# Optimization experiments

Measured on AMD Instinct MI355X. Metric: run time of the kernel, lower is better.

Reference implementation:

```python
import jax, jax.numpy as jnp
import numpy as np


def setup_inputs() -> dict:
    key = jax.random.key(0)
    k1, k2, k3, k4, k5 = jax.random.split(key, 5)
    B, C, H, W = 32, 256, 64, 64
    R = 16  # reduction -> hidden = C // R = 16
    hid = C // R
    return {
        "x": jax.random.normal(k1, (B, C, H, W), dtype=jnp.float32),
        "w1": jax.random.normal(k2, (hid, 1, 1, 1), dtype=jnp.float32) * 0.1,
        "b1": jax.random.normal(k3, (hid,), dtype=jnp.float32) * 0.1,
        "w2": jax.random.normal(k4, (C, hid, 1, 1), dtype=jnp.float32) * 0.1,
        "b2": jax.random.normal(k5, (C,), dtype=jnp.float32) * 0.1,
    }


def reference(x, w1, b1, w2, b2):
    # PositionalAveragePooling: mean over channel dim -> [B, 1, H, W]
    s = jnp.mean(x, axis=1)  # [B, H, W]
    # conv1 (1 -> hid, 1x1): per-position scalar times weight vector + bias
    w1v = w1[:, 0, 0, 0]  # [hid]
    h = jax.nn.relu(s[:, None, :, :] * w1v[None, :, None, None]
                    + b1[None, :, None, None])  # [B, hid, H, W]
    # conv2 (hid -> C, 1x1): pointwise matmul over channel dim
    w2m = w2[:, :, 0, 0]  # [C, hid]
    scale = jax.nn.sigmoid(jnp.einsum("bkhw,ck->bchw", h, w2m)
                           + b2[None, :, None, None])  # [B, C, H, W]
    return x * scale
```

## Files before the change

kernel.cpp:

```cpp
#include <hip/hip_runtime.h>

#define NB 32
#define NC 256
#define NH 64
#define NW 64
#define NK 16
#define HW (NH * NW)

__device__ __forceinline__ float fsig(float z) {
    return __builtin_amdgcn_rcpf(1.0f + __expf(-z));
}

__global__ __launch_bounds__(256, 4) void pse_kernel(
    const float* __restrict__ x,
    const float* __restrict__ w1,
    const float* __restrict__ b1,
    const float* __restrict__ w2,
    const float* __restrict__ b2,
    float* __restrict__ out)
{
    __shared__ float  w2t[NK][NC];
    __shared__ float4 part[16][17];
    __shared__ float4 hv4[NK][16];
    __shared__ float4 s4[16];

    const int t  = threadIdx.x;
    const int cg = t >> 4;
    const int q  = t & 15;

    const int bh = blockIdx.x;
    const int b  = bh >> 6;
    const int h  = bh & 63;

    const size_t base = (size_t)b * NC * HW + (size_t)h * NW;
    const float* __restrict__ xp = x + base;
    float* __restrict__ op       = out + base;

    {
        const float4* w2v = reinterpret_cast<const float4*>(w2);
        #pragma unroll
        for (int r = 0; r < 4; ++r) {
            const int idx = t + (r << 8);
            const float4 v = w2v[idx];
            const int c  = idx >> 2;
            const int k0 = (idx & 3) << 2;
            w2t[k0 + 0][c] = v.x;
            w2t[k0 + 1][c] = v.y;
            w2t[k0 + 2][c] = v.z;
            w2t[k0 + 3][c] = v.w;
        }
    }

    {
        const float* xr = xp + (size_t)(cg << 4) * HW + (q << 2);
        float4 pacc = make_float4(0.f, 0.f, 0.f, 0.f);
        #pragma unroll
        for (int i = 0; i < 16; ++i) {
            const float4 v = *reinterpret_cast<const float4*>(xr + (size_t)i * HW);
            pacc.x += v.x; pacc.y += v.y; pacc.z += v.z; pacc.w += v.w;
        }
        part[cg][q] = pacc;
    }
    __syncthreads();

    if (t < 16) {
        float4 s = make_float4(0.f, 0.f, 0.f, 0.f);
        #pragma unroll
        for (int i = 0; i < 16; ++i) {
            const float4 v = part[i][t];
            s.x += v.x; s.y += v.y; s.z += v.z; s.w += v.w;
        }
        const float inv = 1.0f / (float)NC;
        s.x *= inv; s.y *= inv; s.z *= inv; s.w *= inv;
        s4[t] = s;
    }
    __syncthreads();

    {
        const float4 s  = s4[q];
        const float w1k = w1[cg];
        const float b1k = b1[cg];
        float4 hvv;
        hvv.x = fmaxf(fmaf(s.x, w1k, b1k), 0.f);
        hvv.y = fmaxf(fmaf(s.y, w1k, b1k), 0.f);
        hvv.z = fmaxf(fmaf(s.z, w1k, b1k), 0.f);
        hvv.w = fmaxf(fmaf(s.w, w1k, b1k), 0.f);
        hv4[cg][q] = hvv;
    }
    __syncthreads();

    float4 acc[16];
    #pragma unroll
    for (int i = 0; i < 16; ++i) {
        const float bb = b2[(cg << 4) + i];
        acc[i] = make_float4(bb, bb, bb, bb);
    }

    #pragma unroll
    for (int k = 0; k < NK; ++k) {
        const float4 hk = hv4[k][q];
        const float4* wr = reinterpret_cast<const float4*>(&w2t[k][cg << 4]);
        const float4 wa = wr[0], wb = wr[1], wc = wr[2], wd = wr[3];
        const float wv[16] = {wa.x, wa.y, wa.z, wa.w, wb.x, wb.y, wb.z, wb.w,
                              wc.x, wc.y, wc.z, wc.w, wd.x, wd.y, wd.z, wd.w};
        #pragma unroll
        for (int i = 0; i < 16; ++i) {
            acc[i].x = fmaf(hk.x, wv[i], acc[i].x);
            acc[i].y = fmaf(hk.y, wv[i], acc[i].y);
            acc[i].z = fmaf(hk.z, wv[i], acc[i].z);
            acc[i].w = fmaf(hk.w, wv[i], acc[i].w);
        }
    }

    #pragma unroll
    for (int i = 0; i < 16; ++i) {
        const size_t off = (size_t)((cg << 4) + i) * HW + (q << 2);
        const float4 xv = *reinterpret_cast<const float4*>(xp + off);
        const float4 a  = acc[i];
        float4 r;
        r.x = xv.x * fsig(a.x);
        r.y = xv.y * fsig(a.y);
        r.z = xv.z * fsig(a.z);
        r.w = xv.w * fsig(a.w);
        *reinterpret_cast<float4*>(op + off) = r;
    }
}

extern "C" void kernel_launch(void* const* d_in, const int* in_sizes, int n_in,
                              void* d_out, int out_size, void* d_ws, size_t ws_size,
                              hipStream_t stream) {
    const float* x  = (const float*)d_in[0];
    const float* w1 = (const float*)d_in[1];
    const float* b1 = (const float*)d_in[2];
    const float* w2 = (const float*)d_in[3];
    const float* b2 = (const float*)d_in[4];
    float* out = (float*)d_out;

    dim3 grid(NB * NH);
    dim3 block(256);
    hipLaunchKernelGGL(pse_kernel, grid, block, 0, stream, x, w1, b1, w2, b2, out);
}
```

Before: 255.8 us.

## Keep x tile in registers, use nontemporal loads/stores, split accumulation in halves

Result: faster. 237.7 us (-7.1%).

```diff
diff --git a/kernel.cpp b/kernel.cpp
--- a/kernel.cpp
+++ b/kernel.cpp
@@ -6,6 +6,8 @@
 #define NW 64
 #define NK 16
 #define HW (NH * NW)
+
+typedef float f32x4 __attribute__((ext_vector_type(4)));
 
 __device__ __forceinline__ float fsig(float z) {
     return __builtin_amdgcn_rcpf(1.0f + __expf(-z));
@@ -19,10 +21,11 @@
     const float* __restrict__ b2,
     float* __restrict__ out)
 {
-    __shared__ float  w2t[NK][NC];
-    __shared__ float4 part[16][17];
-    __shared__ float4 hv4[NK][16];
-    __shared__ float4 s4[16];
+    __shared__ float w2t[NK][NC + 4];
+    __shared__ f32x4 part[16][17];
+    __shared__ f32x4 hv4[NK][16];
+    __shared__ f32x4 s4[16];
+    __shared__ float b2s[NC];
 
     const int t  = threadIdx.x;
     const int cg = t >> 4;
@@ -35,13 +38,20 @@
     const size_t base = (size_t)b * NC * HW + (size_t)h * NW;
     const float* __restrict__ xp = x + base;
     float* __restrict__ op       = out + base;
+    const float* __restrict__ xr = xp + (size_t)(cg << 4) * HW + (q << 2);
+
+    f32x4 xv[16];
+    #pragma unroll
+    for (int i = 0; i < 16; ++i)
+        xv[i] = __builtin_nontemporal_load(
+            reinterpret_cast<const f32x4*>(xr + (size_t)i * HW));
 
     {
-        const float4* w2v = reinterpret_cast<const float4*>(w2);
+        const f32x4* __restrict__ w2v = reinterpret_cast<const f32x4*>(w2);
         #pragma unroll
         for (int r = 0; r < 4; ++r) {
             const int idx = t + (r << 8);
-            const float4 v = w2v[idx];
+            const f32x4 v = w2v[idx];
             const int c  = idx >> 2;
             const int k0 = (idx & 3) << 2;
             w2t[k0 + 0][c] = v.x;
@@ -49,38 +59,31 @@
             w2t[k0 + 2][c] = v.z;
             w2t[k0 + 3][c] = v.w;
         }
+        b2s[t] = b2[t];
     }
 
     {
-        const float* xr = xp + (size_t)(cg << 4) * HW + (q << 2);
-        float4 pacc = make_float4(0.f, 0.f, 0.f, 0.f);
+        f32x4 p = (f32x4)(0.f);
         #pragma unroll
-        for (int i = 0; i < 16; ++i) {
-            const float4 v = *reinterpret_cast<const float4*>(xr + (size_t)i * HW);
-            pacc.x += v.x; pacc.y += v.y; pacc.z += v.z; pacc.w += v.w;
-        }
-        part[cg][q] = pacc;
+        for (int i = 0; i < 16; ++i) p += xv[i];
+        part[cg][q] = p;
     }
     __syncthreads();
 
     if (t < 16) {
-        float4 s = make_float4(0.f, 0.f, 0.f, 0.f);
+        f32x4 s = (f32x4)(0.f);
         #pragma unroll
-        for (int i = 0; i < 16; ++i) {
-            const float4 v = part[i][t];
-            s.x += v.x; s.y += v.y; s.z += v.z; s.w += v.w;
-        }
-        const float inv = 1.0f / (float)NC;
-        s.x *= inv; s.y *= inv; s.z *= inv; s.w *= inv;
+        for (int i = 0; i < 16; ++i) s += part[i][t];
+        s *= (1.0f / (float)NC);
         s4[t] = s;
     }
     __syncthreads();
 
     {
-        const float4 s  = s4[q];
+        const f32x4 s  = s4[q];
         const float w1k = w1[cg];
         const float b1k = b1[cg];
-        float4 hvv;
+        f32x4 hvv;
         hvv.x = fmaxf(fmaf(s.x, w1k, b1k), 0.f);
         hvv.y = fmaxf(fmaf(s.y, w1k, b1k), 0.f);
         hvv.z = fmaxf(fmaf(s.z, w1k, b1k), 0.f);
@@ -89,40 +92,42 @@
     }
     __syncthreads();
 
-    float4 acc[16];
     #pragma unroll
-    for (int i = 0; i < 16; ++i) {
-        const float bb = b2[(cg << 4) + i];
-        acc[i] = make_float4(bb, bb, bb, bb);
-    }
+    for (int half = 0; half < 2; ++half) {
+        const int c0 = (cg << 4) + (half << 3);
 
-    #pragma unroll
-    for (int k = 0; k < NK; ++k) {
-        const float4 hk = hv4[k][q];
-        const float4* wr = reinterpret_cast<const float4*>(&w2t[k][cg << 4]);
-        const float4 wa = wr[0], wb = wr[1], wc = wr[2], wd = wr[3];
-        const float wv[16] = {wa.x, wa.y, wa.z, wa.w, wb.x, wb.y, wb.z, wb.w,
-                              wc.x, wc.y, wc.z, wc.w, wd.x, wd.y, wd.z, wd.w};
+        f32x4 acc[8];
         #pragma unroll
-        for (int i = 0; i < 16; ++i) {
-            acc[i].x = fmaf(hk.x, wv[i], acc[i].x);
-            acc[i].y = fmaf(hk.y, wv[i], acc[i].y);
-            acc[i].z = fmaf(hk.z, wv[i], acc[i].z);
-            acc[i].w = fmaf(hk.w, wv[i], acc[i].w);
+        for (int j = 0; j < 8; ++j) acc[j] = (f32x4)(b2s[c0 + j]);
+
+        #pragma unroll
+        for (int k = 0; k < NK; ++k) {
+            const f32x4 hk = hv4[k][q];
+            const f32x4* __restrict__ wr =
+                reinterpret_cast<const f32x4*>(&w2t[k][c0]);
+            const f32x4 wa = wr[0], wb = wr[1];
+            const float wv[8] = {wa.x, wa.y, wa.z, wa.w, wb.x, wb.y, wb.z, wb.w};
+            #pragma unroll
+            for (int j = 0; j < 8; ++j) {
+                acc[j].x = fmaf(hk.x, wv[j], acc[j].x);
+                acc[j].y = fmaf(hk.y, wv[j], acc[j].y);
+                acc[j].z = fmaf(hk.z, wv[j], acc[j].z);
+                acc[j].w = fmaf(hk.w, wv[j], acc[j].w);
+            }
         }
-    }
 
-    #pragma unroll
-    for (int i = 0; i < 16; ++i) {
-        const size_t off = (size_t)((cg << 4) + i) * HW + (q << 2);
-        const float4 xv = *reinterpret_cast<const float4*>(xp + off);
-        const float4 a  = acc[i];
-        float4 r;
-        r.x = xv.x * fsig(a.x);
-        r.y = xv.y * fsig(a.y);
-        r.z = xv.z * fsig(a.z);
-        r.w = xv.w * fsig(a.w);
-        *reinterpret_cast<float4*>(op + off) = r;
+        #pragma unroll
+        for (int j = 0; j < 8; ++j) {
+            const int i = (half << 3) + j;
+            const f32x4 xvv = xv[i];
+            f32x4 r;
+            r.x = xvv.x * fsig(acc[j].x);
+            r.y = xvv.y * fsig(acc[j].y);
+            r.z = xvv.z * fsig(acc[j].z);
+            r.w = xvv.w * fsig(acc[j].w);
+            __builtin_nontemporal_store(r,
+                reinterpret_cast<f32x4*>(op + (size_t)(c0 + j) * HW + (q << 2)));
+        }
     }
 }
 
```
